# Optimization experiments

Hardware: AMD Instinct MI355X
Metric: run time of the kernel (lower is better)

## Reference

```python
import jax, jax.numpy as jnp
import numpy as np

N, E, G = 50000, 800000, 64
IN, H, C, OUT = 128, 4, 64, 128
HC = H * C
NEG, EPS = 0.2, 1e-5


def _glorot(key, shape):
    s = (2.0 / (shape[0] + shape[-1])) ** 0.5
    return jax.random.normal(key, shape, jnp.float32) * s


def setup_inputs() -> dict:
    key = jax.random.key(0)
    ks = iter(jax.random.split(key, 64))
    nk = lambda: next(ks)
    inp = {}
    inp['x'] = jax.random.normal(nk(), (N, IN), jnp.float32)
    inp['edge_index'] = jax.random.randint(nk(), (2, E), 0, N)
    inp['batch'] = jnp.sort(jax.random.randint(nk(), (N,), 0, G))
    # GATv2 layers: (in_dim, heads*out, heads, out_per_head)
    dims = [(IN, HC, H, C), (HC, HC, H, C), (HC, OUT, 1, OUT)]
    for i, (di, do, h, c) in enumerate(dims):
        inp[f'Wl{i}'] = _glorot(nk(), (di, do))
        inp[f'bl{i}'] = jnp.zeros((do,), jnp.float32)
        inp[f'Wr{i}'] = _glorot(nk(), (di, do))
        inp[f'br{i}'] = jnp.zeros((do,), jnp.float32)
        inp[f'a{i}'] = _glorot(nk(), (h, c))
        inp[f'c{i}'] = jnp.zeros((do,), jnp.float32)
    # BatchNorm (eval mode, running stats)
    for i, d in enumerate([HC, HC, OUT]):
        inp[f'g{i}'] = jnp.ones((d,), jnp.float32) + 0.05 * jax.random.normal(nk(), (d,), jnp.float32)
        inp[f'be{i}'] = 0.05 * jax.random.normal(nk(), (d,), jnp.float32)
        inp[f'm{i}'] = 0.05 * jax.random.normal(nk(), (d,), jnp.float32)
        inp[f'v{i}'] = jax.random.uniform(nk(), (d,), jnp.float32, 0.5, 1.5)
    # classifier MLP
    for i, (di, do) in enumerate([(2 * OUT, OUT), (OUT, OUT // 2), (OUT // 2, 1)]):
        inp[f'cw{i}'] = _glorot(nk(), (di, do))
        inp[f'cb{i}'] = jnp.zeros((do,), jnp.float32)
    return inp


def _gat(x, src, dst, Wl, bl, Wr, br, att, bias, heads, ch, concat):
    # GATv2: x_j = lin_l(x)[src] (source/messages), x_i = lin_r(x)[dst] (target)
    n = x.shape[0]
    xl = (x @ Wl + bl).reshape(n, heads, ch)
    xr = (x @ Wr + br).reshape(n, heads, ch)
    e = jax.nn.leaky_relu(xl[src] + xr[dst], NEG)          # [E, H, C]
    s = jnp.einsum('ehc,hc->eh', e, att)                   # per-edge logits
    mx = jnp.full((n, heads), -jnp.inf, s.dtype).at[dst].max(s)
    a = jnp.exp(s - mx[dst])
    den = jnp.zeros((n, heads), s.dtype).at[dst].add(a)
    alpha = a / den[dst]                                   # segment softmax over incoming edges
    out = jnp.zeros((n, heads, ch), x.dtype).at[dst].add(alpha[:, :, None] * xl[src])
    out = out.reshape(n, heads * ch) if concat else out.mean(axis=1)
    return out + bias


def _bn(x, g, b, m, v):
    return (x - m) * g / jnp.sqrt(v + EPS) + b


def _forward(x, Wl0, bl0, Wr0, br0, a0, c0, Wl1, bl1, Wr1, br1, a1, c1,
             Wl2, bl2, Wr2, br2, a2, c2,
             g0, be0, m0, v0, g1, be1, m1, v1, g2, be2, m2, v2,
             cw0, cb0, cw1, cb1, cw2, cb2, src, dst, batch):
    h = jax.nn.elu(_bn(_gat(x, src, dst, Wl0, bl0, Wr0, br0, a0, c0, H, C, True), g0, be0, m0, v0))
    h = jax.nn.elu(_bn(_gat(h, src, dst, Wl1, bl1, Wr1, br1, a1, c1, H, C, True), g1, be1, m1, v1))
    h = _bn(_gat(h, src, dst, Wl2, bl2, Wr2, br2, a2, c2, 1, OUT, False), g2, be2, m2, v2)
    cnt = jnp.zeros((G,), h.dtype).at[batch].add(1.0)
    mean = jnp.zeros((G, OUT), h.dtype).at[batch].add(h) / jnp.maximum(cnt, 1.0)[:, None]
    gmax = jnp.full((G, OUT), -jnp.inf, h.dtype).at[batch].max(h)
    gmax = jnp.where(jnp.isfinite(gmax), gmax, 0.0)
    z = jnp.concatenate([mean, gmax], axis=1)              # [G, 2*OUT]
    z = jax.nn.relu(z @ cw0 + cb0)
    z = jax.nn.relu(z @ cw1 + cb1)
    return z @ cw2 + cb2                                   # [G, 1]


def reference(x, edge_index, batch,
              Wl0, bl0, Wr0, br0, a0, c0, Wl1, bl1, Wr1, br1, a1, c1,
              Wl2, bl2, Wr2, br2, a2, c2,
              g0, be0, m0, v0, g1, be1, m1, v1, g2, be2, m2, v2,
              cw0, cb0, cw1, cb1, cw2, cb2):
    loops = jnp.arange(N, dtype=edge_index.dtype)          # PyG add_self_loops=True
    src = jnp.concatenate([edge_index[0], loops])
    dst = jnp.concatenate([edge_index[1], loops])
    return _forward(x, Wl0, bl0, Wr0, br0, a0, c0, Wl1, bl1, Wr1, br1, a1, c1,
                    Wl2, bl2, Wr2, br2, a2, c2,
                    g0, be0, m0, v0, g1, be1, m1, v1, g2, be2, m2, v2,
                    cw0, cb0, cw1, cb1, cw2, cb2, src, dst, batch)
```

## Files before the change

### kernel.cpp

```cpp
#include <hip/hip_runtime.h>
#include <math.h>

#define NNODES 50000
#define NPAD 50048
#define NEDGES 800000
#define NGRAPH 64
#define NEGS 0.2f
#define BNEPS 1e-5f

typedef _Float16 f16;
typedef f16 f16x2 __attribute__((ext_vector_type(2)));
typedef f16 f16x4 __attribute__((ext_vector_type(4)));
typedef f16 f16x8 __attribute__((ext_vector_type(8)));
typedef float f32x4 __attribute__((ext_vector_type(4)));

__global__ void hist_kernel(const int* __restrict__ ei, int* __restrict__ deg,
                            int nE, int n) {
    int i = blockIdx.x * blockDim.x + threadIdx.x;
    int total = nE + n;
    if (i >= total) return;
    int dst = (i < nE) ? ei[nE + i] : (i - nE);
    atomicAdd(&deg[dst], 1);
}

__global__ __launch_bounds__(256) void scan1_kernel(const int* __restrict__ deg,
                                                    int* __restrict__ bsum, int n) {
    __shared__ int s[256];
    int t = threadIdx.x;
    int idx = blockIdx.x * 1024 + t * 4;
    int v = 0;
    if (idx + 3 < n) {
        int4 d = *(const int4*)&deg[idx];
        v = d.x + d.y + d.z + d.w;
    } else {
        for (int j = 0; j < 4; j++) if (idx + j < n) v += deg[idx + j];
    }
    s[t] = v;
    __syncthreads();
    for (int off = 128; off >= 1; off >>= 1) {
        if (t < off) s[t] += s[t + off];
        __syncthreads();
    }
    if (t == 0) bsum[blockIdx.x] = s[0];
}

__global__ __launch_bounds__(64) void scan2_kernel(int* __restrict__ bsum, int nb) {
    int t = threadIdx.x;
    int v = (t < nb) ? bsum[t] : 0;
    for (int off = 1; off < 64; off <<= 1) {
        int u = __shfl_up(v, off, 64);
        if (t >= off) v += u;
    }
    int ex = __shfl_up(v, 1, 64);
    if (t == 0) ex = 0;
    if (t < nb) bsum[t] = ex;
}

__global__ __launch_bounds__(256) void scan3_kernel(const int* __restrict__ deg,
                                                    const int* __restrict__ bsum,
                                                    int* __restrict__ row_ptr,
                                                    int* __restrict__ cursor, int n) {
    __shared__ int s[256];
    int t = threadIdx.x;
    int idx = blockIdx.x * 1024 + t * 4;
    int d[4] = {0, 0, 0, 0};
    if (idx + 3 < n) {
        int4 dv = *(const int4*)&deg[idx];
        d[0] = dv.x; d[1] = dv.y; d[2] = dv.z; d[3] = dv.w;
    } else {
        for (int j = 0; j < 4; j++) if (idx + j < n) d[j] = deg[idx + j];
    }
    s[t] = d[0] + d[1] + d[2] + d[3];
    __syncthreads();
    for (int off = 1; off < 256; off <<= 1) {
        int v = (t >= off) ? s[t - off] : 0;
        __syncthreads();
        s[t] += v;
        __syncthreads();
    }
    int prefix = bsum[blockIdx.x] + ((t == 0) ? 0 : s[t - 1]);
    for (int j = 0; j < 4; j++) {
        if (idx + j < n) {
            row_ptr[idx + j] = prefix;
            cursor[idx + j] = prefix;
            prefix += d[j];
        }
    }
    if (idx < n && idx + 4 >= n) row_ptr[n] = prefix;
}

__global__ void scatter_kernel(const int* __restrict__ ei, int* __restrict__ cursor,
                               int* __restrict__ col, int nE, int n) {
    int i = blockIdx.x * blockDim.x + threadIdx.x;
    int total = nE + n;
    if (i >= total) return;
    int src, dst;
    if (i < nE) { src = ei[i]; dst = ei[nE + i]; }
    else        { src = i - nE; dst = src; }
    int pos = atomicAdd(&cursor[dst], 1);
    col[pos] = src;
}

__global__ __launch_bounds__(256) void sortadj_kernel(const int* __restrict__ row_ptr,
                                                      int* __restrict__ col, int n) {
    int wv = threadIdx.x >> 6;
    int lane = threadIdx.x & 63;
    int i = (blockIdx.x << 2) + wv;
    if (i >= n) return;
    int lo = row_ptr[i], hi = row_ptr[i + 1];
    int d = hi - lo;
    if (d <= 1) return;
    if (d <= 64) {
        int v = (lane < d) ? col[lo + lane] : 0x7fffffff;
        int rank = 0;
        for (int j = 0; j < d; j++) {
            int u = __shfl(v, j, 64);
            rank += (u < v) || (u == v && j < lane);
        }
        if (lane < d) col[lo + rank] = v;
    } else if (lane == 0) {
        for (int a = lo + 1; a < hi; a++) {
            int v = col[a];
            int b = a - 1;
            while (b >= lo && col[b] > v) { col[b + 1] = col[b]; b--; }
            col[b + 1] = v;
        }
    }
}

__device__ __forceinline__ void packB_one(const float* __restrict__ Wl,
                                          const float* __restrict__ Wr,
                                          f16* __restrict__ Bp, int K, int M,
                                          int idx) {
    int k = idx / (2 * M);
    int nn = idx % (2 * M);
    float v = (nn < M) ? Wl[k * M + nn] : Wr[k * M + (nn - M)];
    int NCG = (2 * M) / 256;
    int ks = k >> 5;
    int quad = (k >> 3) & 3;
    int j = k & 7;
    int lane = quad * 16 + (nn & 15);
    int cg = nn >> 8;
    int tl = (nn >> 4) & 15;
    Bp[((((size_t)ks * NCG + cg) * 16 + tl) * 64 + lane) * 8 + j] = (f16)v;
}

__global__ void prep_kernel(const float* __restrict__ x, f16* __restrict__ xh,
                            const float* __restrict__ Wl0, const float* __restrict__ Wr0,
                            f16* __restrict__ Bp0,
                            const float* __restrict__ Wl1, const float* __restrict__ Wr1,
                            f16* __restrict__ Bp1,
                            const float* __restrict__ Wl2, const float* __restrict__ Wr2,
                            f16* __restrict__ Bp2) {
    int idx = blockIdx.x * blockDim.x + threadIdx.x;
    int cvtN = NNODES * 128 / 4;
    if (idx < cvtN) {
        float4 v = ((const float4*)x)[idx];
        f16x4 o; o.x = (f16)v.x; o.y = (f16)v.y; o.z = (f16)v.z; o.w = (f16)v.w;
        ((f16x4*)xh)[idx] = o;
        return;
    }
    idx -= cvtN;
    if (idx < 128 * 512) { packB_one(Wl0, Wr0, Bp0, 128, 256, idx); return; }
    idx -= 128 * 512;
    if (idx < 256 * 512) { packB_one(Wl1, Wr1, Bp1, 256, 256, idx); return; }
    idx -= 256 * 512;
    if (idx < 256 * 256) { packB_one(Wl2, Wr2, Bp2, 256, 128, idx); }
}

__device__ __forceinline__ void dma16h(const f16* g, f16* l) {
    __builtin_amdgcn_global_load_lds(
        (const __attribute__((address_space(1))) void*)g,
        (__attribute__((address_space(3))) void*)l, 16, 0, 0);
}

template <int K, int M>
__global__ __launch_bounds__(256, 4) void gemm_mfma_kernel(
    const f16* __restrict__ A, const f16* __restrict__ Bp,
    const float* __restrict__ bl, const float* __restrict__ br,
    f16* __restrict__ xlh, f16* __restrict__ xrh, int n) {
    constexpr int KS = K / 32;
    constexpr int NCG = (2 * M) / 256;
    constexpr int TILES = 16;
    __shared__ __align__(16) f16 ldsB[2][8192];

    int w = threadIdx.x >> 6;
    int lane = threadIdx.x & 63;
    int row0 = blockIdx.x * 64 + w * 16;
    int cg = blockIdx.y;
    int col0 = cg * 256;
    int quad = lane >> 4;

    const f16* Arow = A + (size_t)(row0 + (lane & 15)) * K + quad * 8;
    f16x8 av[KS];
#pragma unroll
    for (int ks = 0; ks < KS; ks++) av[ks] = *(const f16x8*)(Arow + ks * 32);

    f32x4 acc[TILES];
#pragma unroll
    for (int t = 0; t < TILES; t++) acc[t] = (f32x4){0.f, 0.f, 0.f, 0.f};

    auto issueB = [&](int ks) {
        size_t slab = ((size_t)ks * NCG + cg) * 8192;
        f16* dst = &ldsB[ks & 1][0];
#pragma unroll
        for (int d = 0; d < 4; d++) {
            int tl = w * 4 + d;
            dma16h(Bp + slab + tl * 512 + lane * 8, dst + tl * 512);
        }
    };

    issueB(0);
    for (int ks = 0; ks < KS; ks++) {
        if (ks + 1 < KS) {
            issueB(ks + 1);
            asm volatile("s_waitcnt vmcnt(4)" ::: "memory");
        } else {
            asm volatile("s_waitcnt vmcnt(0)" ::: "memory");
        }
        asm volatile("s_barrier" ::: "memory");
        const f16* lb = &ldsB[ks & 1][0];
#pragma unroll
        for (int t = 0; t < TILES; t++) {
            f16x8 bv = *(const f16x8*)(lb + t * 512 + lane * 8);
            acc[t] = __builtin_amdgcn_mfma_f32_16x16x32_f16(av[ks], bv, acc[t], 0, 0, 0);
        }
        asm volatile("s_waitcnt lgkmcnt(0)" ::: "memory");
        asm volatile("s_barrier" ::: "memory");
    }

    int rq = quad * 4;
#pragma unroll
    for (int t = 0; t < TILES; t++) {
        int c = col0 + t * 16 + (lane & 15);
        float bias = (c < M) ? bl[c] : br[c - M];
#pragma unroll
        for (int r = 0; r < 4; r++) {
            int row = row0 + rq + r;
            if (row < n) {
                float v = acc[t][r] + bias;
                if (c < M) xlh[(size_t)row * M + c] = (f16)v;
                else       xrh[(size_t)row * M + (c - M)] = (f16)v;
            }
        }
    }
}

template <int H, int C, bool ELU, bool OUTH>
__global__ __launch_bounds__(256) void gat_agg_kernel(
    const f16* __restrict__ xlh, const f16* __restrict__ xrh,
    const float* __restrict__ att, const float* __restrict__ cb,
    const float* __restrict__ bn_g, const float* __restrict__ bn_b,
    const float* __restrict__ bn_m, const float* __restrict__ bn_v,
    const int* __restrict__ row_ptr, const int* __restrict__ col_idx,
    f16* __restrict__ outh, float* __restrict__ outf, int n) {
    constexpr int M = H * C;
    constexpr int VPL = M / 64;
    constexpr int NP = VPL / 2;
    constexpr int EPD = 512 / M;
    constexpr int B = 4;
    constexpr int NDMA = B / EPD;
    constexpr int BUFH = NDMA * 512;

    __shared__ __align__(16) f16 lds[4][2][BUFH];

    int wv = threadIdx.x >> 6;
    int lane = threadIdx.x & 63;
    int wid = (blockIdx.x << 2) + wv;
    if (wid >= n) return;
    const int i = __builtin_amdgcn_readfirstlane(wid);
    const int base = lane * VPL;

    f16x2 xr2[NP], at2[NP];
    float acc[VPL];
#pragma unroll
    for (int p = 0; p < NP; p++) {
        xr2[p] = *(const f16x2*)(xrh + (size_t)i * M + base + 2 * p);
        at2[p].x = (f16)att[base + 2 * p];
        at2[p].y = (f16)att[base + 2 * p + 1];
    }
#pragma unroll
    for (int j = 0; j < VPL; j++) acc[j] = 0.f;
    float den = 0.f;

    f16x2 z2; z2.x = (f16)0.f; z2.y = (f16)0.f;
    f16x2 ns2; ns2.x = (f16)NEGS; ns2.y = (f16)NEGS;

    const int e0 = __builtin_amdgcn_readfirstlane(row_ptr[i]);
    const int e1 = __builtin_amdgcn_readfirstlane(row_ptr[i + 1]);
    const int nb = (e1 - e0 + B - 1) / B;
    const int elast = e1 - 1;

    int nxt[B];
    auto loadcols = [&](int kk) {
#pragma unroll
        for (int b = 0; b < B; b++) {
            int idx = e0 + kk * B + b;
            nxt[b] = col_idx[min(idx, elast)];
        }
    };
    auto issue = [&](int buf) {
        f16* lbase = &lds[wv][buf][0];
#pragma unroll
        for (int d = 0; d < NDMA; d++) {
            int sel = (EPD == 2) ? (lane >> 5) : (lane >> 4);
            int r = nxt[EPD * d + sel];
            const f16* g = xlh + (size_t)r * M + ((lane & (64 / EPD - 1)) << 3);
            dma16h(g, lbase + d * 512);
        }
    };

    loadcols(0);
    issue(0);
    if (nb > 1) loadcols(1);

    for (int k = 0; k < nb; k++) {
        bool more = (k + 1 < nb);
        if (more) {
            issue((k + 1) & 1);
            if (NDMA == 2)
                asm volatile("s_waitcnt vmcnt(2)" ::: "memory");
            else
                asm volatile("s_waitcnt vmcnt(1)" ::: "memory");
        } else {
            asm volatile("s_waitcnt vmcnt(0)" ::: "memory");
        }
        if (k + 2 < nb) loadcols(k + 2);

        const f16* lb = &lds[wv][k & 1][0];
        const int ebase = e0 + k * B;
        f16x4 xv4[B];
        float sc[B];
#pragma unroll
        for (int b = 0; b < B; b++) {
            const f16* rowp = (EPD == 2)
                ? lb + (b >> 1) * 512 + (b & 1) * 256 + lane * 4
                : lb + (b & 3) * 128 + lane * 2;
            if (VPL == 4) {
                xv4[b] = *(const f16x4*)rowp;
            } else {
                f16x2 t = *(const f16x2*)rowp;
                xv4[b].x = t.x; xv4[b].y = t.y;
            }
            float s = 0.f;
#pragma unroll
            for (int p = 0; p < NP; p++) {
                f16x2 xp;
                xp.x = (p == 0) ? xv4[b].x : xv4[b].z;
                xp.y = (p == 0) ? xv4[b].y : xv4[b].w;
                f16x2 t = xp + xr2[p];
                f16x2 lk = __builtin_elementwise_max(t, z2) +
                           ns2 * __builtin_elementwise_min(t, z2);
                s = __builtin_amdgcn_fdot2(lk, at2[p], s, false);
            }
            sc[b] = s;
        }
        constexpr int RED = (H == 4) ? 8 : 32;
#pragma unroll
        for (int off = 1; off <= RED; off <<= 1)
#pragma unroll
            for (int b = 0; b < B; b++) sc[b] += __shfl_xor(sc[b], off, 64);
#pragma unroll
        for (int b = 0; b < B; b++) {
            float w = (ebase + b < e1) ? __expf(sc[b]) : 0.f;
            den += w;
            acc[0] += w * (float)xv4[b].x;
            acc[1] += w * (float)xv4[b].y;
            if (VPL == 4) {
                acc[2] += w * (float)xv4[b].z;
                acc[3] += w * (float)xv4[b].w;
            }
        }
    }

    float inv = 1.0f / den;
    float ov[VPL];
#pragma unroll
    for (int j = 0; j < VPL; j++) {
        int hc = base + j;
        float val = acc[j] * inv + cb[hc];
        val = (val - bn_m[hc]) * bn_g[hc] / sqrtf(bn_v[hc] + BNEPS) + bn_b[hc];
        if (ELU) val = (val > 0.f) ? val : expm1f(val);
        ov[j] = val;
    }
    if (OUTH) {
        f16* op = outh + (size_t)i * M + base;
        if (VPL == 4) {
            f16x4 v; v.x = (f16)ov[0]; v.y = (f16)ov[1];
            v.z = (f16)ov[2]; v.w = (f16)ov[3];
            *(f16x4*)op = v;
        } else {
            f16x2 v; v.x = (f16)ov[0]; v.y = (f16)ov[1];
            *(f16x2*)op = v;
        }
    } else {
        float* op = outf + (size_t)i * M + base;
        if (VPL == 4) {
            float4 v; v.x = ov[0]; v.y = ov[1]; v.z = ov[2]; v.w = ov[3];
            *(float4*)op = v;
        } else {
            float2 v; v.x = ov[0]; v.y = ov[1];
            *(float2*)op = v;
        }
    }
}

__device__ __forceinline__ int lower_bound_i(const int* a, int n, int v) {
    int lo = 0, hi = n;
    while (lo < hi) {
        int m = (lo + hi) >> 1;
        if (a[m] < v) lo = m + 1; else hi = m;
    }
    return lo;
}

__global__ __launch_bounds__(512) void pool_kernel(
    const float* __restrict__ h, const int* __restrict__ batch,
    float* __restrict__ sum_out, float* __restrict__ max_out,
    float* __restrict__ cnt, int n) {
    int g = blockIdx.x;
    int tid = threadIdx.x;
    int ch = tid & 127;
    int r = tid >> 7;

    int lo = lower_bound_i(batch, n, g);
    int hi = lower_bound_i(batch, n, g + 1);

    float sum = 0.f, mx = -INFINITY;
    for (int i = lo + r; i < hi; i += 4) {
        float v = h[(size_t)i * 128 + ch];
        sum += v;
        mx = fmaxf(mx, v);
    }
    __shared__ float ssum[512], smax[512];
    ssum[tid] = sum; smax[tid] = mx;
    __syncthreads();
    if (r == 0) {
        sum = ssum[ch] + ssum[128 + ch] + ssum[256 + ch] + ssum[384 + ch];
        mx = fmaxf(fmaxf(smax[ch], smax[128 + ch]),
                   fmaxf(smax[256 + ch], smax[384 + ch]));
        sum_out[g * 128 + ch] = sum;
        max_out[g * 128 + ch] = mx;
        if (ch == 0) cnt[g] = (float)(hi - lo);
    }
}

__global__ __launch_bounds__(128) void mlp_kernel(
    const float* __restrict__ sum_in, const float* __restrict__ max_in,
    const float* __restrict__ cnt, const float* __restrict__ cw0,
    const float* __restrict__ cb0, const float* __restrict__ cw1,
    const float* __restrict__ cb1, const float* __restrict__ cw2,
    const float* __restrict__ cb2, float* __restrict__ out) {
    int g = blockIdx.x;
    int t = threadIdx.x;
    __shared__ float z[256];
    __shared__ float z1[128];

    float c = cnt[g];
    float inv = 1.0f / fmaxf(c, 1.0f);
    z[t] = sum_in[g * 128 + t] * inv;
    float mx = max_in[g * 128 + t];
    if (!isfinite(mx)) mx = 0.f;
    z[128 + t] = mx;
    __syncthreads();

    float a = cb0[t];
    for (int k = 0; k < 256; k++) a += z[k] * cw0[k * 128 + t];
    z1[t] = fmaxf(a, 0.f);
    __syncthreads();

    if (t < 64) {
        float b = cb1[t];
        for (int k = 0; k < 128; k++) b += z1[k] * cw1[k * 64 + t];
        float p = fmaxf(b, 0.f) * cw2[t];
#pragma unroll
        for (int off = 32; off >= 1; off >>= 1) p += __shfl_xor(p, off, 64);
        if (t == 0) out[g] = p + cb2[0];
    }
}

extern "C" void kernel_launch(void* const* d_in, const int* in_sizes, int n_in,
                              void* d_out, int out_size, void* d_ws, size_t ws_size,
                              hipStream_t stream) {
    const float* x = (const float*)d_in[0];
    const int* ei = (const int*)d_in[1];
    const int* batch = (const int*)d_in[2];
    const float* Wl0 = (const float*)d_in[3];
    const float* bl0 = (const float*)d_in[4];
    const float* Wr0 = (const float*)d_in[5];
    const float* br0 = (const float*)d_in[6];
    const float* a0 = (const float*)d_in[7];
    const float* c0 = (const float*)d_in[8];
    const float* Wl1 = (const float*)d_in[9];
    const float* bl1 = (const float*)d_in[10];
    const float* Wr1 = (const float*)d_in[11];
    const float* br1 = (const float*)d_in[12];
    const float* a1 = (const float*)d_in[13];
    const float* c1 = (const float*)d_in[14];
    const float* Wl2 = (const float*)d_in[15];
    const float* bl2 = (const float*)d_in[16];
    const float* Wr2 = (const float*)d_in[17];
    const float* br2 = (const float*)d_in[18];
    const float* a2 = (const float*)d_in[19];
    const float* c2 = (const float*)d_in[20];
    const float* g0 = (const float*)d_in[21];
    const float* be0 = (const float*)d_in[22];
    const float* m0 = (const float*)d_in[23];
    const float* v0 = (const float*)d_in[24];
    const float* g1 = (const float*)d_in[25];
    const float* be1 = (const float*)d_in[26];
    const float* m1 = (const float*)d_in[27];
    const float* v1 = (const float*)d_in[28];
    const float* g2 = (const float*)d_in[29];
    const float* be2 = (const float*)d_in[30];
    const float* m2 = (const float*)d_in[31];
    const float* v2 = (const float*)d_in[32];
    const float* cw0 = (const float*)d_in[33];
    const float* cb0 = (const float*)d_in[34];
    const float* cw1 = (const float*)d_in[35];
    const float* cb1 = (const float*)d_in[36];
    const float* cw2 = (const float*)d_in[37];
    const float* cb2 = (const float*)d_in[38];
    float* out = (float*)d_out;

    const int N = NNODES, E = NEDGES, G = NGRAPH;
    char* ws = (char*)d_ws;
    size_t off = 0;
    auto alloc = [&](size_t bytes) -> void* {
        void* p = ws + off;
        off += (bytes + 255) & ~(size_t)255;
        return p;
    };
    f16* xh = (f16*)alloc((size_t)NPAD * 128 * 2);
    f16* h16 = (f16*)alloc((size_t)NPAD * 256 * 2);
    f16* xlh = (f16*)alloc((size_t)NPAD * 256 * 2);
    f16* xrh = (f16*)alloc((size_t)NPAD * 256 * 2);
    float* h2 = (float*)alloc((size_t)N * 128 * 4);
    f16* Bp0 = (f16*)alloc((size_t)128 * 512 * 2);
    f16* Bp1 = (f16*)alloc((size_t)256 * 512 * 2);
    f16* Bp2 = (f16*)alloc((size_t)256 * 256 * 2);
    int* deg = (int*)alloc((size_t)N * 4);
    int* row_ptr = (int*)alloc((size_t)(N + 1) * 4);
    int* cursor = (int*)alloc((size_t)N * 4);
    int* col_idx = (int*)alloc((size_t)(E + N) * 4);
    int* bsum = (int*)alloc((size_t)64 * 4);
    float* mean_acc = (float*)alloc((size_t)G * 128 * 4);
    float* gmax_f = (float*)alloc((size_t)G * 128 * 4);
    float* cnt = (float*)alloc((size_t)G * 4);
    (void)ws_size; (void)n_in; (void)in_sizes; (void)out_size;

    hipMemsetAsync(deg, 0, (size_t)N * 4, stream);

    int totE = E + N;
    int ntiles = (N + 1023) / 1024;
    hist_kernel<<<(totE + 255) / 256, 256, 0, stream>>>(ei, deg, E, N);
    scan1_kernel<<<ntiles, 256, 0, stream>>>(deg, bsum, N);
    scan2_kernel<<<1, 64, 0, stream>>>(bsum, ntiles);
    scan3_kernel<<<ntiles, 256, 0, stream>>>(deg, bsum, row_ptr, cursor, N);
    scatter_kernel<<<(totE + 255) / 256, 256, 0, stream>>>(ei, cursor, col_idx, E, N);
    sortadj_kernel<<<(N + 3) / 4, 256, 0, stream>>>(row_ptr, col_idx, N);

    int prepN = N * 128 / 4 + 128 * 512 + 256 * 512 + 256 * 256;
    prep_kernel<<<(prepN + 255) / 256, 256, 0, stream>>>(
        x, xh, Wl0, Wr0, Bp0, Wl1, Wr1, Bp1, Wl2, Wr2, Bp2);

    int gblocks = NPAD / 64;
    int agg_grid = (N + 3) / 4;

    gemm_mfma_kernel<128, 256><<<dim3(gblocks, 2), 256, 0, stream>>>(
        xh, Bp0, bl0, br0, xlh, xrh, N);
    gat_agg_kernel<4, 64, true, true><<<agg_grid, 256, 0, stream>>>(
        xlh, xrh, a0, c0, g0, be0, m0, v0, row_ptr, col_idx, h16, nullptr, N);

    gemm_mfma_kernel<256, 256><<<dim3(gblocks, 2), 256, 0, stream>>>(
        h16, Bp1, bl1, br1, xlh, xrh, N);
    gat_agg_kernel<4, 64, true, true><<<agg_grid, 256, 0, stream>>>(
        xlh, xrh, a1, c1, g1, be1, m1, v1, row_ptr, col_idx, h16, nullptr, N);

    gemm_mfma_kernel<256, 128><<<dim3(gblocks, 1), 256, 0, stream>>>(
        h16, Bp2, bl2, br2, xlh, xrh, N);
    gat_agg_kernel<1, 128, false, false><<<agg_grid, 256, 0, stream>>>(
        xlh, xrh, a2, c2, g2, be2, m2, v2, row_ptr, col_idx, nullptr, h2, N);

    pool_kernel<<<G, 512, 0, stream>>>(h2, batch, mean_acc, gmax_f, cnt, N);
    mlp_kernel<<<G, 128, 0, stream>>>(mean_acc, gmax_f, cnt, cw0, cb0, cw1, cb1, cw2, cb2, out);
}
```

Measured before the change: 680.6 us.

## Compute two 16-row A tiles per wave to reuse each LDS B fragment

Each GEMM block now covers 128 rows instead of 64, so every wave keeps two sets of A fragments and two accumulator arrays. Each B fragment read from LDS then feeds two MFMAs. This halves the number of blocks and the B slab traffic per output row. The cost is higher register pressure, so launch bounds drop from 4 to 2 blocks per CU, which lowers occupancy and reduces how much latency can be hidden.

```diff
diff --git a/kernel.cpp b/kernel.cpp
--- a/kernel.cpp
+++ b/kernel.cpp
@@ -175,7 +175,7 @@
 }
 
 template <int K, int M>
-__global__ __launch_bounds__(256, 4) void gemm_mfma_kernel(
+__global__ __launch_bounds__(256, 2) void gemm_mfma_kernel(
     const f16* __restrict__ A, const f16* __restrict__ Bp,
     const float* __restrict__ bl, const float* __restrict__ br,
     f16* __restrict__ xlh, f16* __restrict__ xrh, int n) {
@@ -186,19 +186,27 @@
 
     int w = threadIdx.x >> 6;
     int lane = threadIdx.x & 63;
-    int row0 = blockIdx.x * 64 + w * 16;
+    int rowBase = blockIdx.x * 128;
+    int rt0 = rowBase + w * 16;
+    int rt1 = rowBase + 64 + w * 16;
     int cg = blockIdx.y;
     int col0 = cg * 256;
     int quad = lane >> 4;
 
-    const f16* Arow = A + (size_t)(row0 + (lane & 15)) * K + quad * 8;
-    f16x8 av[KS];
-#pragma unroll
-    for (int ks = 0; ks < KS; ks++) av[ks] = *(const f16x8*)(Arow + ks * 32);
-
-    f32x4 acc[TILES];
-#pragma unroll
-    for (int t = 0; t < TILES; t++) acc[t] = (f32x4){0.f, 0.f, 0.f, 0.f};
+    const f16* Arow0 = A + (size_t)(rt0 + (lane & 15)) * K + quad * 8;
+    const f16* Arow1 = A + (size_t)(rt1 + (lane & 15)) * K + quad * 8;
+    f16x8 av[2][KS];
+#pragma unroll
+    for (int ks = 0; ks < KS; ks++) {
+        av[0][ks] = *(const f16x8*)(Arow0 + ks * 32);
+        av[1][ks] = *(const f16x8*)(Arow1 + ks * 32);
+    }
+
+    f32x4 acc[2][TILES];
+#pragma unroll
+    for (int r = 0; r < 2; r++)
+#pragma unroll
+        for (int t = 0; t < TILES; t++) acc[r][t] = (f32x4){0.f, 0.f, 0.f, 0.f};
 
     auto issueB = [&](int ks) {
         size_t slab = ((size_t)ks * NCG + cg) * 8192;
@@ -223,7 +231,8 @@
 #pragma unroll
         for (int t = 0; t < TILES; t++) {
             f16x8 bv = *(const f16x8*)(lb + t * 512 + lane * 8);
-            acc[t] = __builtin_amdgcn_mfma_f32_16x16x32_f16(av[ks], bv, acc[t], 0, 0, 0);
+            acc[0][t] = __builtin_amdgcn_mfma_f32_16x16x32_f16(av[0][ks], bv, acc[0][t], 0, 0, 0);
+            acc[1][t] = __builtin_amdgcn_mfma_f32_16x16x32_f16(av[1][ks], bv, acc[1][t], 0, 0, 0);
         }
         asm volatile("s_waitcnt lgkmcnt(0)" ::: "memory");
         asm volatile("s_barrier" ::: "memory");
@@ -231,16 +240,20 @@
 
     int rq = quad * 4;
 #pragma unroll
-    for (int t = 0; t < TILES; t++) {
-        int c = col0 + t * 16 + (lane & 15);
-        float bias = (c < M) ? bl[c] : br[c - M];
-#pragma unroll
-        for (int r = 0; r < 4; r++) {
-            int row = row0 + rq + r;
-            if (row < n) {
-                float v = acc[t][r] + bias;
-                if (c < M) xlh[(size_t)row * M + c] = (f16)v;
-                else       xrh[(size_t)row * M + (c - M)] = (f16)v;
+    for (int rr = 0; rr < 2; rr++) {
+        int rbase = (rr == 0) ? rt0 : rt1;
+#pragma unroll
+        for (int t = 0; t < TILES; t++) {
+            int c = col0 + t * 16 + (lane & 15);
+            float bias = (c < M) ? bl[c] : br[c - M];
+#pragma unroll
+            for (int r = 0; r < 4; r++) {
+                int row = rbase + rq + r;
+                if (row < n) {
+                    float v = acc[rr][t][r] + bias;
+                    if (c < M) xlh[(size_t)row * M + c] = (f16)v;
+                    else       xrh[(size_t)row * M + (c - M)] = (f16)v;
+                }
             }
         }
     }
@@ -564,7 +577,7 @@
     prep_kernel<<<(prepN + 255) / 256, 256, 0, stream>>>(
         x, xh, Wl0, Wr0, Bp0, Wl1, Wr1, Bp1, Wl2, Wr2, Bp2);
 
-    int gblocks = NPAD / 64;
+    int gblocks = NPAD / 128;
     int agg_grid = (N + 3) / 4;
 
     gemm_mfma_kernel<128, 256><<<dim3(gblocks, 2), 256, 0, stream>>>(
```

Measured after the change: 721.5 us. +6.0%, slower.
